# Kernel optimization log

Measured on AMD Instinct MI355X. Metric: run time of the kernel, lower is better.

Reference implementation:

```python
import jax, jax.numpy as jnp
import numpy as np

N_NODES = 100000
N_EDGES = 1600000
D = 128          # h_size == feature_representation_size
N_CLASSES = 2
N_GRAPHS = 64


def setup_inputs() -> dict:
    key = jax.random.key(0)
    ks = jax.random.split(key, 8)
    scale = 1.0 / np.sqrt(D)
    x = jax.random.normal(ks[0], (N_NODES, D), jnp.float32)
    edge_index = jax.random.randint(ks[1], (2, N_EDGES), 0, N_NODES, dtype=jnp.int64)
    batch = jnp.sort(jax.random.randint(ks[2], (N_NODES,), 0, N_GRAPHS, dtype=jnp.int64))
    W0 = jax.random.normal(ks[3], (D, D), jnp.float32) * scale
    W1 = jax.random.normal(ks[4], (D, D), jnp.float32) * scale
    W2 = jax.random.normal(ks[5], (D, D), jnp.float32) * scale
    Wf = jax.random.normal(ks[6], (D, N_CLASSES), jnp.float32) * scale
    return dict(
        x=x, edge_index=edge_index, batch=batch,
        W0=W0, b0=jnp.zeros((D,), jnp.float32),
        W1=W1, b1=jnp.zeros((D,), jnp.float32),
        W2=W2, b2=jnp.zeros((D,), jnp.float32),
        Wf=Wf, bf=jnp.zeros((N_CLASSES,), jnp.float32),
    )


def gcn_norm(edge_index, num_nodes):
    # add self loops, symmetric normalization D^{-1/2} A_hat D^{-1/2}
    src, dst = edge_index[0], edge_index[1]
    loop = jnp.arange(num_nodes, dtype=src.dtype)
    src = jnp.concatenate([src, loop])
    dst = jnp.concatenate([dst, loop])
    ew = jnp.ones(src.shape[0], jnp.float32)
    deg = jax.ops.segment_sum(ew, dst, num_segments=num_nodes)
    dinv = jnp.where(deg > 0, jax.lax.rsqrt(deg), 0.0)
    norm = dinv[src] * dinv[dst]  # [E+N]
    return src, dst, norm


def gcn_conv(h, W, b, src, dst, norm, num_nodes):
    h = h @ W                                   # linear transform
    msg = h[src] * norm[:, None]                # gather + scale over edges
    out = jax.ops.segment_sum(msg, dst, num_segments=num_nodes)  # scatter-add
    return out + b


def reference(x, edge_index, batch, W0, b0, W1, b1, W2, b2, Wf, bf):
    n = x.shape[0]
    src, dst, norm = gcn_norm(edge_index, n)
    h = jax.nn.relu(gcn_conv(x, W0, b0, src, dst, norm, n))
    h = jax.nn.relu(gcn_conv(h, W1, b1, src, dst, norm, n))
    h = gcn_conv(h, W2, b2, src, dst, norm, n)  # last layer, no relu
    pooled = jax.ops.segment_max(h, batch, num_segments=N_GRAPHS)  # global max pool
    return pooled @ Wf + bf
```

## Files before the change

### kernel.cpp

```cpp
#include <hip/hip_runtime.h>
#include <hip/hip_bf16.h>
#include <hip/hip_fp16.h>
#include <float.h>

#define D 128
#define NGRAPHS 64
#define BKSHIFT 9
#define BKNODES 512
#define MAXBK 256
#define PCH 2048

typedef _Float16 h8 __attribute__((ext_vector_type(8)));
typedef float f4 __attribute__((ext_vector_type(4)));

__device__ __forceinline__ unsigned fkey(float f){
  unsigned u = __float_as_uint(f);
  return (u & 0x80000000u) ? ~u : (u | 0x80000000u);
}
__device__ __forceinline__ float funkey(unsigned k){
  unsigned u = (k & 0x80000000u) ? (k ^ 0x80000000u) : ~k;
  return __uint_as_float(u);
}

__device__ __forceinline__ void wcvt_pair(const float* __restrict__ W,
    _Float16* __restrict__ dstp, int pair, int lane){
  int quad = lane >> 4;
  int n    = lane & 15;
  int k0 = pair >> 3;
  int tt = pair & 7;
  _Float16 v[8];
  #pragma unroll
  for (int j = 0; j < 8; j++){
    int k = k0 * 32 + quad * 8 + j;
    v[j] = (_Float16)W[k * 128 + 16 * tt + n];
  }
  *(uint4*)&dstp[((size_t)pair * 64 + lane) * 8] = *(uint4*)v;
}

__global__ __launch_bounds__(256) void k_wcvt0(const float* __restrict__ W0,
    _Float16* __restrict__ Wsw, int* __restrict__ bcnt){
  if (blockIdx.x == 0 && threadIdx.x < MAXBK) bcnt[threadIdx.x] = 0;
  int lane = threadIdx.x & 63;
  int pair = blockIdx.x * 4 + (threadIdx.x >> 6);
  wcvt_pair(W0, Wsw, pair, lane);
}

#define HCH 4096
__global__ __launch_bounds__(256) void k_mega(
    const float* __restrict__ x, const _Float16* __restrict__ Wsw0,
    _Float16* __restrict__ C, int M, int gb,
    const int* __restrict__ dst, int* __restrict__ bcnt, int E, int nh,
    const float* __restrict__ W1, const float* __restrict__ W2,
    _Float16* __restrict__ Wsw12){
  __shared__ __align__(16) char smraw[4 * 16 * 136 * 2];
  int bid = blockIdx.x;
  if (bid < gb){
    _Float16 (*lds)[136] = (_Float16(*)[136])(smraw + (threadIdx.x >> 6) * 16 * 136 * 2);
    int lane = threadIdx.x & 63;
    int quad = lane >> 4;
    int l15  = lane & 15;
    int m0 = bid * 64 + (threadIdx.x >> 6) * 16;
    if (m0 >= M) return;
    f4 acc[8] = {};
    h8 af[4];
    const float* arow = x + (size_t)(m0 + l15) * D;
    #pragma unroll
    for (int k0 = 0; k0 < 4; k0++){
      float4 a = *(const float4*)&arow[k0 * 32 + quad * 8];
      float4 b = *(const float4*)&arow[k0 * 32 + quad * 8 + 4];
      __half2 p0 = __floats2half2_rn(a.x, a.y);
      __half2 p1 = __floats2half2_rn(a.z, a.w);
      __half2 p2 = __floats2half2_rn(b.x, b.y);
      __half2 p3 = __floats2half2_rn(b.z, b.w);
      union { uint4 u; h8 v; } cv;
      cv.u.x = *(unsigned*)&p0; cv.u.y = *(unsigned*)&p1;
      cv.u.z = *(unsigned*)&p2; cv.u.w = *(unsigned*)&p3;
      af[k0] = cv.v;
    }
    #pragma unroll
    for (int k0 = 0; k0 < 4; k0++){
      #pragma unroll
      for (int t = 0; t < 8; t++){
        h8 bf = *(const h8*)&Wsw0[((size_t)(k0 * 8 + t) * 64 + lane) * 8];
        acc[t] = __builtin_amdgcn_mfma_f32_16x16x32_f16(af[k0], bf, acc[t], 0, 0, 0);
      }
    }
    #pragma unroll
    for (int t = 0; t < 8; t++){
      #pragma unroll
      for (int r = 0; r < 4; r++)
        lds[quad * 4 + r][t * 16 + l15] = (_Float16)acc[t][r];
    }
    #pragma unroll
    for (int it = 0; it < 4; it++){
      int idx = it * 64 + lane;
      int row = idx >> 4;
      int ch  = idx & 15;
      *(uint4*)&C[(size_t)(m0 + row) * D + ch * 8] = *(uint4*)&lds[row][ch * 8];
    }
    return;
  }
  bid -= gb;
  if (bid < nh){
    int* h = (int*)smraw;
    int t = threadIdx.x;
    for (int i = t; i < MAXBK; i += 256) h[i] = 0;
    __syncthreads();
    int e0 = bid * HCH;
    #pragma unroll
    for (int j = 0; j < HCH / 256; j++){
      int e = e0 + t + j * 256;
      if (e < E) atomicAdd(&h[dst[e] >> BKSHIFT], 1);
    }
    __syncthreads();
    for (int i = t; i < MAXBK; i += 256) if (h[i]) atomicAdd(&bcnt[i], h[i]);
    return;
  }
  bid -= nh;
  const float* W = (bid < 2) ? W1 : W2;
  _Float16* dstp = Wsw12 + ((bid < 2) ? 0 : 16384);
  int pbase = (bid & 1) * 16;
  int lane = threadIdx.x & 63;
  for (int pp = (threadIdx.x >> 6); pp < 16; pp += 4)
    wcvt_pair(W, dstp, pbase + pp, lane);
}

__global__ __launch_bounds__(256) void k_bscan(const int* __restrict__ bcnt,
    int* __restrict__ bOff, int* __restrict__ bCur, int* __restrict__ row_ptr,
    unsigned* __restrict__ pk, int nbk, int N, int E){
  __shared__ int sh[256];
  int t = threadIdx.x;
  for (int i = t; i < NGRAPHS * D; i += 256) pk[i] = 0u;
  int v = (t < nbk) ? bcnt[t] : 0;
  sh[t] = v; __syncthreads();
  for (int off = 1; off < 256; off <<= 1){
    int x = (t >= off) ? sh[t - off] : 0;
    __syncthreads();
    sh[t] += x;
    __syncthreads();
  }
  if (t < nbk){ int ex = sh[t] - v; bOff[t] = ex; bCur[t] = ex; }
  if (t == 0){ bOff[nbk] = E; row_ptr[N] = E; }
}

__global__ __launch_bounds__(256) void k_part(const int* __restrict__ src,
    const int* __restrict__ dst, int* __restrict__ bCur,
    uint2* __restrict__ epart, int E){
  __shared__ int scnt[MAXBK], soff[MAXBK], sbase[MAXBK], scur[MAXBK];
  __shared__ int stmp[256];
  __shared__ uint2 stage[PCH];
  int t = threadIdx.x;
  int e0 = blockIdx.x * PCH;
  int eN = E - e0; if (eN > PCH) eN = PCH;
  for (int i = t; i < MAXBK; i += 256){ scnt[i] = 0; scur[i] = 0; }
  __syncthreads();
  uint2 mye[PCH / 256];
  #pragma unroll
  for (int j = 0; j < PCH / 256; j++){
    int e = e0 + t + j * 256;
    if (e < E){
      mye[j].x = (unsigned)src[e];
      mye[j].y = (unsigned)dst[e];
      atomicAdd(&scnt[mye[j].y >> BKSHIFT], 1);
    }
  }
  __syncthreads();
  int v = scnt[t];
  stmp[t] = v; __syncthreads();
  for (int off = 1; off < 256; off <<= 1){
    int x = (t >= off) ? stmp[t - off] : 0;
    __syncthreads();
    stmp[t] += x;
    __syncthreads();
  }
  soff[t] = stmp[t] - v;
  if (v > 0) sbase[t] = atomicAdd(&bCur[t], v);
  __syncthreads();
  #pragma unroll
  for (int j = 0; j < PCH / 256; j++){
    int e = e0 + t + j * 256;
    if (e < E){
      int b = mye[j].y >> BKSHIFT;
      int l = atomicAdd(&scur[b], 1);
      stage[soff[b] + l] = mye[j];
    }
  }
  __syncthreads();
  for (int j = t; j < eN; j += 256){
    uint2 ed = stage[j];
    int b = (int)(ed.y >> BKSHIFT);
    epart[(size_t)sbase[b] + (j - soff[b])] = ed;
  }
}

__global__ __launch_bounds__(256) void k_bfill(const uint2* __restrict__ epart,
    const int* __restrict__ bOff, int* __restrict__ row_ptr,
    int* __restrict__ col, float* __restrict__ dinv, int N){
  __shared__ int hc[BKNODES], off[BKNODES], cur[BKNODES];
  __shared__ int stmp[256];
  int b = blockIdx.x, t = threadIdx.x;
  int base = bOff[b], cntE = bOff[b + 1] - base;
  int node0 = b << BKSHIFT;
  int nloc = N - node0; if (nloc > BKNODES) nloc = BKNODES;
  for (int i = t; i < BKNODES; i += 256) hc[i] = 0;
  __syncthreads();
  for (int j = t; j < cntE; j += 256){
    uint2 ed = epart[(size_t)base + j];
    atomicAdd(&hc[ed.y - node0], 1);
  }
  __syncthreads();
  int a0 = hc[2 * t], a1 = hc[2 * t + 1];
  int s = a0 + a1;
  stmp[t] = s; __syncthreads();
  for (int o = 1; o < 256; o <<= 1){
    int x = (t >= o) ? stmp[t - o] : 0;
    __syncthreads();
    stmp[t] += x;
    __syncthreads();
  }
  int ex = stmp[t] - s;
  off[2 * t] = ex; off[2 * t + 1] = ex + a0;
  __syncthreads();
  for (int i = t; i < nloc; i += 256){
    row_ptr[node0 + i] = base + off[i];
    dinv[node0 + i]    = rsqrtf((float)hc[i] + 1.0f);
    cur[i] = off[i];
  }
  __syncthreads();
  for (int j = t; j < cntE; j += 256){
    uint2 ed = epart[(size_t)base + j];
    int p = atomicAdd(&cur[ed.y - node0], 1);
    col[base + p] = (int)ed.x;
  }
}

__device__ __forceinline__ void accm(float* acc, uint4 u, float w){
  union { uint4 u; _Float16 h[8]; } cv;
  cv.u = u;
  #pragma unroll
  for (int k = 0; k < 8; k++)
    acc[k] += (float)cv.h[k] * w;
}

__global__ __launch_bounds__(256) void k_agg(const __half* __restrict__ t,
    const int* __restrict__ row_ptr, const int* __restrict__ col,
    const float* __restrict__ dinv, const float* __restrict__ bias,
    __half* __restrict__ outh, int relu, int N){
  int node = blockIdx.x * 4 + (threadIdx.x >> 6);
  if (node >= N) return;
  int lane = threadIdx.x & 63;
  int way  = lane >> 4;
  int cg   = (lane & 15) * 8;
  float di = dinv[node];
  int beg = row_ptr[node], end = row_ptr[node + 1];
  float acc[8] = {0.f,0.f,0.f,0.f,0.f,0.f,0.f,0.f};
  int j = beg + way;
  for (; j + 12 < end; j += 16){
    int s0 = col[j], s1 = col[j + 4], s2 = col[j + 8], s3 = col[j + 12];
    float w0 = dinv[s0] * di;
    float w1 = dinv[s1] * di;
    float w2 = dinv[s2] * di;
    float w3 = dinv[s3] * di;
    uint4 u0 = *(const uint4*)&t[(size_t)s0 * D + cg];
    uint4 u1 = *(const uint4*)&t[(size_t)s1 * D + cg];
    uint4 u2 = *(const uint4*)&t[(size_t)s2 * D + cg];
    uint4 u3 = *(const uint4*)&t[(size_t)s3 * D + cg];
    accm(acc, u0, w0);
    accm(acc, u1, w1);
    accm(acc, u2, w2);
    accm(acc, u3, w3);
  }
  for (; j < end; j += 4){
    int s = col[j];
    float w = dinv[s] * di;
    uint4 u = *(const uint4*)&t[(size_t)s * D + cg];
    accm(acc, u, w);
  }
  #pragma unroll
  for (int k = 0; k < 8; k++){
    acc[k] += __shfl_xor(acc[k], 16, 64);
    acc[k] += __shfl_xor(acc[k], 32, 64);
  }
  if (way == 0){
    uint4 su = *(const uint4*)&t[(size_t)node * D + cg];
    union { uint4 u; _Float16 h[8]; } sv; sv.u = su;
    float dii = di * di;
    float4 b0 = *(const float4*)&bias[cg];
    float4 b1 = *(const float4*)&bias[cg + 4];
    float bb[8] = {b0.x, b0.y, b0.z, b0.w, b1.x, b1.y, b1.z, b1.w};
    float o[8];
    #pragma unroll
    for (int k = 0; k < 8; k++)
      o[k] = acc[k] + (float)sv.h[k] * dii + bb[k];
    if (relu){
      #pragma unroll
      for (int k = 0; k < 8; k++) o[k] = fmaxf(o[k], 0.f);
    }
    __half2 p0 = __floats2half2_rn(o[0], o[1]);
    __half2 p1 = __floats2half2_rn(o[2], o[3]);
    __half2 p2 = __floats2half2_rn(o[4], o[5]);
    __half2 p3 = __floats2half2_rn(o[6], o[7]);
    uint4 u;
    u.x = *(unsigned*)&p0; u.y = *(unsigned*)&p1;
    u.z = *(unsigned*)&p2; u.w = *(unsigned*)&p3;
    *(uint4*)&outh[(size_t)node * D + cg] = u;
  }
}

__global__ __launch_bounds__(256) void k_aggw(const __half* __restrict__ t,
    const int* __restrict__ row_ptr, const int* __restrict__ col,
    const float* __restrict__ dinv, const _Float16* __restrict__ Wsw,
    const float* __restrict__ bias, _Float16* __restrict__ outh,
    const int* __restrict__ batch, unsigned* __restrict__ pk,
    int relu, int dopool, int N){
  __shared__ _Float16 lds[4][16][136];
  int wave = threadIdx.x >> 6;
  int lane = threadIdx.x & 63;
  int way  = lane >> 4;
  int l15  = lane & 15;
  int cg   = l15 * 8;
  int n0 = blockIdx.x * 64;
  int m0 = n0 + wave * 16;
  bool act = (m0 < N);
  if (act){
    for (int i = 0; i < 16; i++){
      int node = m0 + i;
      float di = dinv[node];
      int beg = row_ptr[node], end = row_ptr[node + 1];
      float acc[8] = {0.f,0.f,0.f,0.f,0.f,0.f,0.f,0.f};
      int j = beg + way;
      for (; j + 12 < end; j += 16){
        int s0 = col[j], s1 = col[j + 4], s2 = col[j + 8], s3 = col[j + 12];
        float w0 = dinv[s0] * di;
        float w1 = dinv[s1] * di;
        float w2 = dinv[s2] * di;
        float w3 = dinv[s3] * di;
        uint4 u0 = *(const uint4*)&t[(size_t)s0 * D + cg];
        uint4 u1 = *(const uint4*)&t[(size_t)s1 * D + cg];
        uint4 u2 = *(const uint4*)&t[(size_t)s2 * D + cg];
        uint4 u3 = *(const uint4*)&t[(size_t)s3 * D + cg];
        accm(acc, u0, w0);
        accm(acc, u1, w1);
        accm(acc, u2, w2);
        accm(acc, u3, w3);
      }
      for (; j < end; j += 4){
        int s = col[j];
        float w = dinv[s] * di;
        uint4 u = *(const uint4*)&t[(size_t)s * D + cg];
        accm(acc, u, w);
      }
      #pragma unroll
      for (int k = 0; k < 8; k++){
        acc[k] += __shfl_xor(acc[k], 16, 64);
        acc[k] += __shfl_xor(acc[k], 32, 64);
      }
      if (way == 0){
        uint4 su = *(const uint4*)&t[(size_t)node * D + cg];
        union { uint4 u; _Float16 h[8]; } sv; sv.u = su;
        float dii = di * di;
        _Float16 o[8];
        #pragma unroll
        for (int k = 0; k < 8; k++)
          o[k] = (_Float16)(acc[k] + (float)sv.h[k] * dii);
        *(uint4*)&lds[wave][i][cg] = *(uint4*)o;
      }
    }
    h8 af[4];
    #pragma unroll
    for (int k0 = 0; k0 < 4; k0++)
      af[k0] = *(const h8*)&lds[wave][l15][k0 * 32 + way * 8];
    f4 c[8] = {};
    #pragma unroll
    for (int k0 = 0; k0 < 4; k0++){
      #pragma unroll
      for (int tt = 0; tt < 8; tt++){
        h8 bfr = *(const h8*)&Wsw[((size_t)(k0 * 8 + tt) * 64 + lane) * 8];
        c[tt] = __builtin_amdgcn_mfma_f32_16x16x32_f16(af[k0], bfr, c[tt], 0, 0, 0);
      }
    }
    #pragma unroll
    for (int tt = 0; tt < 8; tt++){
      float b = bias[tt * 16 + l15];
      #pragma unroll
      for (int r = 0; r < 4; r++){
        float v = c[tt][r] + b;
        if (relu) v = fmaxf(v, 0.f);
        lds[wave][way * 4 + r][tt * 16 + l15] = (_Float16)v;
      }
    }
    if (!dopool){
      #pragma unroll
      for (int it = 0; it < 4; it++){
        int idx = it * 64 + lane;
        int row = idx >> 4;
        int ch  = idx & 15;
        if (m0 + row < N)
          *(uint4*)&outh[(size_t)(m0 + row) * D + ch * 8] = *(uint4*)&lds[wave][row][ch * 8];
      }
    }
  }
  if (dopool){
    __syncthreads();
    if (threadIdx.x < 128){
      int d = threadIdx.x;
      int nEnd = N - n0; if (nEnd > 64) nEnd = 64;
      float cur = -FLT_MAX;
      int curg = batch[n0];
      for (int n = 0; n < nEnd; n++){
        int g = batch[n0 + n];
        if (g != curg){ atomicMax(&pk[curg * D + d], fkey(cur)); cur = -FLT_MAX; curg = g; }
        cur = fmaxf(cur, (float)lds[n >> 4][n & 15][d]);
      }
      atomicMax(&pk[curg * D + d], fkey(cur));
    }
  }
}

__global__ __launch_bounds__(128) void k_final(const unsigned* __restrict__ pk,
    const float* __restrict__ Wf, const float* __restrict__ bf,
    float* __restrict__ out){
  int t = threadIdx.x;
  int g = t >> 1, c = t & 1;
  float s = bf[c];
  for (int k = 0; k < D; k++)
    s += funkey(pk[g * D + k]) * Wf[k * 2 + c];
  out[g * 2 + c] = s;
}

extern "C" void kernel_launch(void* const* d_in, const int* in_sizes, int n_in,
                              void* d_out, int out_size, void* d_ws, size_t ws_size,
                              hipStream_t stream){
  const float* x   = (const float*)d_in[0];
  const int*   ei  = (const int*)d_in[1];
  const int*   bat = (const int*)d_in[2];
  const float* W0  = (const float*)d_in[3];
  const float* b0  = (const float*)d_in[4];
  const float* W1  = (const float*)d_in[5];
  const float* b1  = (const float*)d_in[6];
  const float* W2  = (const float*)d_in[7];
  const float* b2  = (const float*)d_in[8];
  const float* Wf  = (const float*)d_in[9];
  const float* bf  = (const float*)d_in[10];
  int N = in_sizes[0] / D;
  int E = in_sizes[1] / 2;
  const int* srcp = ei;
  const int* dstp = ei + E;
  int nbk   = (N + BKNODES - 1) / BKNODES;
  int npart = (E + PCH - 1) / PCH;
  int nh    = (E + HCH - 1) / HCH;
  int gb    = (N + 63) / 64;

  char* p = (char*)d_ws;
  auto alloc = [&](size_t bytes)->char*{
    char* r = p; p += (bytes + 255) & ~(size_t)255; return r;
  };
  float*     dinv    = (float*)alloc((size_t)N * 4);
  int*       row_ptr = (int*)alloc((size_t)(N + 1) * 4);
  int*       col     = (int*)alloc((size_t)E * 4);
  uint2*     epart   = (uint2*)alloc((size_t)E * 8);
  _Float16*  tmp     = (_Float16*)alloc((size_t)N * D * 2);
  _Float16*  tmp2    = (_Float16*)alloc((size_t)N * D * 2);
  _Float16*  Wsw     = (_Float16*)alloc((size_t)3 * 16384 * 2);
  unsigned*  pk      = (unsigned*)alloc((size_t)NGRAPHS * D * 4);
  int*       bcnt    = (int*)alloc((size_t)MAXBK * 4);
  int*       bOff    = (int*)alloc((size_t)(MAXBK + 1) * 4);
  int*       bCur    = (int*)alloc((size_t)MAXBK * 4);

  k_wcvt0<<<8, 256, 0, stream>>>(W0, Wsw, bcnt);
  k_mega<<<gb + nh + 4, 256, 0, stream>>>(x, Wsw, tmp, N, gb,
      dstp, bcnt, E, nh, W1, W2, Wsw + 16384);
  k_bscan<<<1, 256, 0, stream>>>(bcnt, bOff, bCur, row_ptr, pk, nbk, N, E);
  k_part<<<npart, 256, 0, stream>>>(srcp, dstp, bCur, epart, E);
  k_bfill<<<nbk, 256, 0, stream>>>(epart, bOff, row_ptr, col, dinv, N);

  int ablocks = (N + 3) / 4;
  int fblocks = (N + 63) / 64;
  k_agg<<<ablocks, 256, 0, stream>>>((const __half*)tmp, row_ptr, col, dinv, b0, (__half*)tmp2, 1, N);
  k_aggw<<<fblocks, 256, 0, stream>>>((const __half*)tmp2, row_ptr, col, dinv,
      Wsw + 16384, b1, tmp, (const int*)nullptr, (unsigned*)nullptr, 1, 0, N);
  k_aggw<<<fblocks, 256, 0, stream>>>((const __half*)tmp, row_ptr, col, dinv,
      Wsw + 32768, b2, (_Float16*)nullptr, bat, pk, 0, 1, N);
  k_final<<<1, 128, 0, stream>>>(pk, Wf, bf, (float*)d_out);
}
```

Before: 458.5 us.

## Drop bucket-scan kernel and split aggregate-transform blocks across 16-node tiles

Removes the single-block k_bscan launch: the bucket offset scan is now recomputed redundantly inside every k_part and k_bfill block, and the pk and bCur zeroing moves into k_wcvt0. Separately, the fused aggregate+matmul kernel now processes 16 nodes per block, with each wave gathering 4 rows and computing 2 of the 8 output column tiles, instead of one wave handling 16 nodes and all 8 tiles. This is meant to cut one launch and serialisation point and to raise block count and balance for the gather phase. The cost is redundant 256-wide scans in every block, extra block barriers, and more pooling atomics, since there are now four times as many blocks.

Result: faster. 404.9 us (-11.7%).

```diff
diff --git a/kernel.cpp b/kernel.cpp
--- a/kernel.cpp
+++ b/kernel.cpp
@@ -38,8 +38,15 @@
 }
 
 __global__ __launch_bounds__(256) void k_wcvt0(const float* __restrict__ W0,
-    _Float16* __restrict__ Wsw, int* __restrict__ bcnt){
-  if (blockIdx.x == 0 && threadIdx.x < MAXBK) bcnt[threadIdx.x] = 0;
+    _Float16* __restrict__ Wsw, int* __restrict__ bcnt, int* __restrict__ bCur,
+    unsigned* __restrict__ pk){
+  if (blockIdx.x == 0 && threadIdx.x < MAXBK){
+    bcnt[threadIdx.x] = 0;
+    bCur[threadIdx.x] = 0;
+  }
+  #pragma unroll
+  for (int i = 0; i < 4; i++)
+    pk[blockIdx.x * 1024 + i * 256 + threadIdx.x] = 0u;
   int lane = threadIdx.x & 63;
   int pair = blockIdx.x * 4 + (threadIdx.x >> 6);
   wcvt_pair(W0, Wsw, pair, lane);
@@ -125,31 +132,23 @@
     wcvt_pair(W, dstp, pbase + pp, lane);
 }
 
-__global__ __launch_bounds__(256) void k_bscan(const int* __restrict__ bcnt,
-    int* __restrict__ bOff, int* __restrict__ bCur, int* __restrict__ row_ptr,
-    unsigned* __restrict__ pk, int nbk, int N, int E){
-  __shared__ int sh[256];
-  int t = threadIdx.x;
-  for (int i = t; i < NGRAPHS * D; i += 256) pk[i] = 0u;
-  int v = (t < nbk) ? bcnt[t] : 0;
-  sh[t] = v; __syncthreads();
-  for (int off = 1; off < 256; off <<= 1){
-    int x = (t >= off) ? sh[t - off] : 0;
-    __syncthreads();
-    sh[t] += x;
-    __syncthreads();
-  }
-  if (t < nbk){ int ex = sh[t] - v; bOff[t] = ex; bCur[t] = ex; }
-  if (t == 0){ bOff[nbk] = E; row_ptr[N] = E; }
-}
-
 __global__ __launch_bounds__(256) void k_part(const int* __restrict__ src,
-    const int* __restrict__ dst, int* __restrict__ bCur,
-    uint2* __restrict__ epart, int E){
+    const int* __restrict__ dst, const int* __restrict__ bcnt,
+    int* __restrict__ bCur, uint2* __restrict__ epart, int E){
   __shared__ int scnt[MAXBK], soff[MAXBK], sbase[MAXBK], scur[MAXBK];
   __shared__ int stmp[256];
   __shared__ uint2 stage[PCH];
   int t = threadIdx.x;
+  int bv = bcnt[t];
+  stmp[t] = bv; __syncthreads();
+  for (int off = 1; off < 256; off <<= 1){
+    int x = (t >= off) ? stmp[t - off] : 0;
+    __syncthreads();
+    stmp[t] += x;
+    __syncthreads();
+  }
+  int boffl = stmp[t] - bv;
+  __syncthreads();
   int e0 = blockIdx.x * PCH;
   int eN = E - e0; if (eN > PCH) eN = PCH;
   for (int i = t; i < MAXBK; i += 256){ scnt[i] = 0; scur[i] = 0; }
@@ -174,7 +173,7 @@
     __syncthreads();
   }
   soff[t] = stmp[t] - v;
-  if (v > 0) sbase[t] = atomicAdd(&bCur[t], v);
+  if (v > 0) sbase[t] = boffl + atomicAdd(&bCur[t], v);
   __syncthreads();
   #pragma unroll
   for (int j = 0; j < PCH / 256; j++){
@@ -194,12 +193,23 @@
 }
 
 __global__ __launch_bounds__(256) void k_bfill(const uint2* __restrict__ epart,
-    const int* __restrict__ bOff, int* __restrict__ row_ptr,
-    int* __restrict__ col, float* __restrict__ dinv, int N){
+    const int* __restrict__ bcnt, int* __restrict__ row_ptr,
+    int* __restrict__ col, float* __restrict__ dinv, int N, int E){
   __shared__ int hc[BKNODES], off[BKNODES], cur[BKNODES];
   __shared__ int stmp[256];
   int b = blockIdx.x, t = threadIdx.x;
-  int base = bOff[b], cntE = bOff[b + 1] - base;
+  int bv = bcnt[t];
+  stmp[t] = bv; __syncthreads();
+  for (int o = 1; o < 256; o <<= 1){
+    int x = (t >= o) ? stmp[t - o] : 0;
+    __syncthreads();
+    stmp[t] += x;
+    __syncthreads();
+  }
+  int cntE = bcnt[b];
+  int base = stmp[b] - cntE;
+  __syncthreads();
+  if (b == (int)gridDim.x - 1 && t == 0) row_ptr[N] = E;
   int node0 = b << BKSHIFT;
   int nloc = N - node0; if (nloc > BKNODES) nloc = BKNODES;
   for (int i = t; i < BKNODES; i += 256) hc[i] = 0;
@@ -307,24 +317,23 @@
   }
 }
 
-__global__ __launch_bounds__(256) void k_aggw(const __half* __restrict__ t,
+__global__ __launch_bounds__(256) void k_aggw2(const __half* __restrict__ t,
     const int* __restrict__ row_ptr, const int* __restrict__ col,
     const float* __restrict__ dinv, const _Float16* __restrict__ Wsw,
     const float* __restrict__ bias, _Float16* __restrict__ outh,
     const int* __restrict__ batch, unsigned* __restrict__ pk,
     int relu, int dopool, int N){
-  __shared__ _Float16 lds[4][16][136];
+  __shared__ _Float16 A[16][136];
   int wave = threadIdx.x >> 6;
   int lane = threadIdx.x & 63;
   int way  = lane >> 4;
   int l15  = lane & 15;
   int cg   = l15 * 8;
-  int n0 = blockIdx.x * 64;
-  int m0 = n0 + wave * 16;
-  bool act = (m0 < N);
-  if (act){
-    for (int i = 0; i < 16; i++){
-      int node = m0 + i;
+  int m0 = blockIdx.x * 16;
+  for (int i = 0; i < 4; i++){
+    int row = wave * 4 + i;
+    int node = m0 + row;
+    if (node < N){
       float di = dinv[node];
       int beg = row_ptr[node], end = row_ptr[node + 1];
       float acc[8] = {0.f,0.f,0.f,0.f,0.f,0.f,0.f,0.f};
@@ -363,54 +372,56 @@
         #pragma unroll
         for (int k = 0; k < 8; k++)
           o[k] = (_Float16)(acc[k] + (float)sv.h[k] * dii);
-        *(uint4*)&lds[wave][i][cg] = *(uint4*)o;
-      }
-    }
-    h8 af[4];
-    #pragma unroll
-    for (int k0 = 0; k0 < 4; k0++)
-      af[k0] = *(const h8*)&lds[wave][l15][k0 * 32 + way * 8];
-    f4 c[8] = {};
-    #pragma unroll
-    for (int k0 = 0; k0 < 4; k0++){
-      #pragma unroll
-      for (int tt = 0; tt < 8; tt++){
-        h8 bfr = *(const h8*)&Wsw[((size_t)(k0 * 8 + tt) * 64 + lane) * 8];
-        c[tt] = __builtin_amdgcn_mfma_f32_16x16x32_f16(af[k0], bfr, c[tt], 0, 0, 0);
-      }
-    }
-    #pragma unroll
-    for (int tt = 0; tt < 8; tt++){
-      float b = bias[tt * 16 + l15];
-      #pragma unroll
-      for (int r = 0; r < 4; r++){
-        float v = c[tt][r] + b;
-        if (relu) v = fmaxf(v, 0.f);
-        lds[wave][way * 4 + r][tt * 16 + l15] = (_Float16)v;
-      }
-    }
-    if (!dopool){
-      #pragma unroll
-      for (int it = 0; it < 4; it++){
-        int idx = it * 64 + lane;
-        int row = idx >> 4;
-        int ch  = idx & 15;
-        if (m0 + row < N)
-          *(uint4*)&outh[(size_t)(m0 + row) * D + ch * 8] = *(uint4*)&lds[wave][row][ch * 8];
-      }
-    }
-  }
-  if (dopool){
-    __syncthreads();
+        *(uint4*)&A[row][cg] = *(uint4*)o;
+      }
+    } else if (way == 0){
+      uint4 z = {0u, 0u, 0u, 0u};
+      *(uint4*)&A[row][cg] = z;
+    }
+  }
+  __syncthreads();
+  h8 af[4];
+  #pragma unroll
+  for (int k0 = 0; k0 < 4; k0++)
+    af[k0] = *(const h8*)&A[l15][k0 * 32 + way * 8];
+  __syncthreads();
+  f4 c[2] = {};
+  #pragma unroll
+  for (int k0 = 0; k0 < 4; k0++){
+    #pragma unroll
+    for (int tti = 0; tti < 2; tti++){
+      int tt = wave * 2 + tti;
+      h8 bfr = *(const h8*)&Wsw[((size_t)(k0 * 8 + tt) * 64 + lane) * 8];
+      c[tti] = __builtin_amdgcn_mfma_f32_16x16x32_f16(af[k0], bfr, c[tti], 0, 0, 0);
+    }
+  }
+  #pragma unroll
+  for (int tti = 0; tti < 2; tti++){
+    int tt = wave * 2 + tti;
+    float b = bias[tt * 16 + l15];
+    #pragma unroll
+    for (int r = 0; r < 4; r++){
+      float v = c[tti][r] + b;
+      if (relu) v = fmaxf(v, 0.f);
+      A[way * 4 + r][tt * 16 + l15] = (_Float16)v;
+    }
+  }
+  __syncthreads();
+  if (!dopool){
+    int row = threadIdx.x >> 4;
+    int ch  = threadIdx.x & 15;
+    if (m0 + row < N)
+      *(uint4*)&outh[(size_t)(m0 + row) * D + ch * 8] = *(uint4*)&A[row][ch * 8];
+  } else {
     if (threadIdx.x < 128){
       int d = threadIdx.x;
-      int nEnd = N - n0; if (nEnd > 64) nEnd = 64;
+      int nEnd = N - m0; if (nEnd > 16) nEnd = 16;
       float cur = -FLT_MAX;
-      int curg = batch[n0];
+      int curg = batch[m0];
       for (int n = 0; n < nEnd; n++){
-        int g = batch[n0 + n];
+        int g = batch[m0 + n];
         if (g != curg){ atomicMax(&pk[curg * D + d], fkey(cur)); cur = -FLT_MAX; curg = g; }
-        cur = fmaxf(cur, (float)lds[n >> 4][n & 15][d]);
+        cur = fmaxf(cur, (float)A[n][d]);
       }
       atomicMax(&pk[curg * D + d], fkey(cur));
     }
@@ -464,22 +475,20 @@
   _Float16*  Wsw     = (_Float16*)alloc((size_t)3 * 16384 * 2);
   unsigned*  pk      = (unsigned*)alloc((size_t)NGRAPHS * D * 4);
   int*       bcnt    = (int*)alloc((size_t)MAXBK * 4);
-  int*       bOff    = (int*)alloc((size_t)(MAXBK + 1) * 4);
   int*       bCur    = (int*)alloc((size_t)MAXBK * 4);
 
-  k_wcvt0<<<8, 256, 0, stream>>>(W0, Wsw, bcnt);
+  k_wcvt0<<<8, 256, 0, stream>>>(W0, Wsw, bcnt, bCur, pk);
   k_mega<<<gb + nh + 4, 256, 0, stream>>>(x, Wsw, tmp, N, gb,
       dstp, bcnt, E, nh, W1, W2, Wsw + 16384);
-  k_bscan<<<1, 256, 0, stream>>>(bcnt, bOff, bCur, row_ptr, pk, nbk, N, E);
-  k_part<<<npart, 256, 0, stream>>>(srcp, dstp, bCur, epart, E);
-  k_bfill<<<nbk, 256, 0, stream>>>(epart, bOff, row_ptr, col, dinv, N);
+  k_part<<<npart, 256, 0, stream>>>(srcp, dstp, bcnt, bCur, epart, E);
+  k_bfill<<<nbk, 256, 0, stream>>>(epart, bcnt, row_ptr, col, dinv, N, E);
 
   int ablocks = (N + 3) / 4;
-  int fblocks = (N + 63) / 64;
+  int fblocks = (N + 15) / 16;
   k_agg<<<ablocks, 256, 0, stream>>>((const __half*)tmp, row_ptr, col, dinv, b0, (__half*)tmp2, 1, N);
-  k_aggw<<<fblocks, 256, 0, stream>>>((const __half*)tmp2, row_ptr, col, dinv,
+  k_aggw2<<<fblocks, 256, 0, stream>>>((const __half*)tmp2, row_ptr, col, dinv,
       Wsw + 16384, b1, tmp, (const int*)nullptr, (unsigned*)nullptr, 1, 0, N);
-  k_aggw<<<fblocks, 256, 0, stream>>>((const __half*)tmp, row_ptr, col, dinv,
+  k_aggw2<<<fblocks, 256, 0, stream>>>((const __half*)tmp, row_ptr, col, dinv,
       Wsw + 32768, b2, (_Float16*)nullptr, bat, pk, 0, 1, N);
   k_final<<<1, 128, 0, stream>>>(pk, Wf, bf, (float*)d_out);
 }
```
